# Performance work log

Measured on AMD Instinct MI355X. Metric: run time of the kernel, lower is better.

Reference implementation:

```python
import jax, jax.numpy as jnp
import numpy as np

N = 50000      # nodes
E = 800000     # edges (avg degree 16)
D = 64         # node feature dim
DE = 32        # edge feature dim
H = 256        # MLP hidden dim


def setup_inputs() -> dict:
    key = jax.random.key(0)
    k0, k1, k2, k3, k4 = jax.random.split(key, 5)
    x = jax.random.normal(k0, (N, D), dtype=jnp.float32)
    edge_index = jax.random.randint(k1, (2, E), 0, N)
    edge_attr = jax.random.normal(k2, (E, DE), dtype=jnp.float32)
    fan_in1 = 2 * D + DE  # 160
    W1 = jax.random.normal(k3, (fan_in1, H), dtype=jnp.float32) / np.float32(np.sqrt(fan_in1))
    b1 = jnp.zeros((H,), dtype=jnp.float32)
    W2 = jax.random.normal(k4, (H, D), dtype=jnp.float32) / np.float32(np.sqrt(H))
    b2 = jnp.zeros((D,), dtype=jnp.float32)
    return {"x": x, "edge_index": edge_index, "edge_attr": edge_attr,
            "W1": W1, "b1": b1, "W2": W2, "b2": b2}


def reference(x, edge_index, edge_attr, W1, b1, W2, b2):
    row, col = edge_index[0], edge_index[1]
    # gather endpoint features + edge features -> [E, 2D+DE]
    feats = jnp.concatenate([x[row], x[col], edge_attr], axis=-1)
    # MLP: Linear -> ReLU -> Linear
    h = jax.nn.relu(feats @ W1 + b1)          # [E, H]
    out = h @ W2 + b2                          # [E, D]
    # scatter-max aggregate by source node (row), dim_size = N
    agg = jax.ops.segment_max(out, row, num_segments=N)  # [N, D]
    # PyG's old scatter_('max') zero-fills empty slots
    agg = jnp.where(jnp.isneginf(agg), jnp.float32(0.0), agg)
    return (agg, out)
```

## Files before the change

### kernel.cpp

```cpp
#include <hip/hip_runtime.h>
#include <hip/hip_bf16.h>
#include <math.h>

#define NNODES 50000
#define NEDGES 800000
#define CHUNKS (NEDGES / 32)
#define NBLK 256
#define GWAVES (NBLK * 16)

using short8 = __attribute__((ext_vector_type(8))) short;
using f32x4  = __attribute__((ext_vector_type(4))) float;
using f32x16 = __attribute__((ext_vector_type(16))) float;
using u32x4  = __attribute__((ext_vector_type(4))) unsigned;

__device__ __forceinline__ short f2b(float v) {
    return __builtin_bit_cast(short, __float2bfloat16(v));
}
__device__ __forceinline__ unsigned cvt2(float a, float b) {
    return (unsigned)(unsigned short)f2b(a) | ((unsigned)(unsigned short)f2b(b) << 16);
}

__global__ void prep_all(const float* __restrict__ x, short* __restrict__ xb,
                         const float* __restrict__ W1, const float* __restrict__ W2,
                         short* __restrict__ wpk, const int* __restrict__ ei,
                         unsigned* __restrict__ cnt)
{
    int b = blockIdx.x;
    if (b < 3125) {
        int i = b * 256 + threadIdx.x;
        float4 v = reinterpret_cast<const float4*>(x)[i];
        short4 o;
        o.x = f2b(v.x); o.y = f2b(v.y); o.z = f2b(v.z); o.w = f2b(v.w);
        reinterpret_cast<short4*>(xb)[i] = o;
    } else if (b < 6250) {
        int e = (b - 3125) * 256 + threadIdx.x;
        atomicAdd(&cnt[ei[e]], 1u);
    } else {
        int i = (b - 6250) * 256 + threadIdx.x;
        if (i < 40960) {
            int k = i >> 8, n = i & 255;
            int lane = (n & 31) + (((k >> 3) & 1) << 5);
            wpk[(((n >> 5) * 10 + (k >> 4)) * 64 + lane) * 8 + (k & 7)] = f2b(W1[i]);
        }
        if (i < 16384) {
            int k = i >> 6, n = i & 63;
            int lane = (n & 31) + (((k >> 3) & 1) << 5);
            wpk[40960 + (((n >> 5) * 16 + (k >> 4)) * 64 + lane) * 8 + (k & 7)] = f2b(W2[i]);
        }
    }
}

__global__ __launch_bounds__(1024)
void csr_scan1(const unsigned* __restrict__ cnt, unsigned* __restrict__ offs,
               unsigned* __restrict__ bsum) {
    __shared__ unsigned sbuf[1024];
    int t = threadIdx.x, i = blockIdx.x * 1024 + t;
    unsigned v = (i < NNODES) ? cnt[i] : 0u;
    sbuf[t] = v;
    __syncthreads();
    for (int off = 1; off < 1024; off <<= 1) {
        unsigned add = (t >= off) ? sbuf[t - off] : 0u;
        __syncthreads();
        sbuf[t] += add;
        __syncthreads();
    }
    if (i < NNODES) offs[i] = sbuf[t];
    if (t == 1023) bsum[blockIdx.x] = sbuf[1023];
}

__global__ void csr_scan2(unsigned* __restrict__ bsum) {
    int t = threadIdx.x;
    unsigned v = (t < 49) ? bsum[t] : 0u;
    unsigned orig = v;
    for (int off = 1; off < 64; off <<= 1) {
        unsigned n = __shfl_up(v, off, 64);
        if (t >= off) v += n;
    }
    if (t < 49) bsum[t] = v - orig;
}

__global__ __launch_bounds__(1024)
void csr_scan3(const unsigned* __restrict__ cnt, unsigned* __restrict__ offs,
               const unsigned* __restrict__ bsum) {
    int i = blockIdx.x * 1024 + threadIdx.x;
    if (i < NNODES)       offs[i] = offs[i] - cnt[i] + bsum[blockIdx.x];
    else if (i == NNODES) offs[i] = NEDGES;
}

__global__ void csr_place(const int* __restrict__ ei, const unsigned* __restrict__ offs,
                          unsigned* __restrict__ cur, unsigned* __restrict__ elist) {
    int e = blockIdx.x * 256 + threadIdx.x;
    if (e < NEDGES) {
        int r = ei[e];
        unsigned p = offs[r] + atomicAdd(&cur[r], 1u);
        elist[p] = (unsigned)e;
    }
}

__global__ __launch_bounds__(1024, 4)
void edgeconv_main(const short* __restrict__ xb, const int* __restrict__ ei,
                   const float* __restrict__ ea, const short* __restrict__ wpk,
                   const float* __restrict__ b1, const float* __restrict__ b2,
                   float* __restrict__ outbuf)
{
    __shared__ short wlds[57344];

    for (int i = threadIdx.x; i < 7168; i += 1024)
        reinterpret_cast<short8*>(wlds)[i] = reinterpret_cast<const short8*>(wpk)[i];
    __syncthreads();

    const short* w1s = wlds;
    const short* w2s = wlds + 40960;
    const int lane = threadIdx.x & 63;
    const int wave = threadIdx.x >> 6;
    const int l32 = lane & 31, hi = lane >> 5;
    const int gw = blockIdx.x * 16 + wave;

    for (int c = gw; c < CHUNKS; c += GWAVES) {
        const int ebase = c * 32;
        const int e = ebase + l32;
        const int r = ei[e], cc = ei[NEDGES + e];

        short8 fx[10];
        #pragma unroll
        for (int ks = 0; ks < 4; ++ks)
            fx[ks] = *reinterpret_cast<const short8*>(xb + r * 64 + ks * 16 + hi * 8);
        #pragma unroll
        for (int ks = 0; ks < 4; ++ks)
            fx[4 + ks] = *reinterpret_cast<const short8*>(xb + cc * 64 + ks * 16 + hi * 8);
        #pragma unroll
        for (int ks = 0; ks < 2; ++ks) {
            const float4* p = reinterpret_cast<const float4*>(ea + e * 32 + ks * 16 + hi * 8);
            float4 a = p[0], b = p[1];
            u32x4 uu;
            uu[0] = cvt2(a.x, a.y); uu[1] = cvt2(a.z, a.w);
            uu[2] = cvt2(b.x, b.y); uu[3] = cvt2(b.z, b.w);
            fx[8 + ks] = __builtin_bit_cast(short8, uu);
        }

        f32x16 acc2[2];
        #pragma unroll
        for (int t2 = 0; t2 < 2; ++t2)
            #pragma unroll
            for (int g = 0; g < 4; ++g) {
                float4 bb = *reinterpret_cast<const float4*>(b2 + t2 * 32 + g * 8 + hi * 4);
                acc2[t2][g * 4 + 0] = bb.x; acc2[t2][g * 4 + 1] = bb.y;
                acc2[t2][g * 4 + 2] = bb.z; acc2[t2][g * 4 + 3] = bb.w;
            }

        #pragma unroll 1
        for (int t = 0; t < 8; ++t) {
            f32x16 acc1;
            #pragma unroll
            for (int g = 0; g < 4; ++g) {
                float4 bb = *reinterpret_cast<const float4*>(b1 + t * 32 + g * 8 + hi * 4);
                acc1[g * 4 + 0] = bb.x; acc1[g * 4 + 1] = bb.y;
                acc1[g * 4 + 2] = bb.z; acc1[g * 4 + 3] = bb.w;
            }
            #pragma unroll
            for (int ks = 0; ks < 10; ++ks) {
                short8 wf = *reinterpret_cast<const short8*>(
                    w1s + ((t * 10 + ks) * 64 + lane) * 8);
                acc1 = __builtin_amdgcn_mfma_f32_32x32x16_bf16(wf, fx[ks], acc1, 0, 0, 0);
            }
            #pragma unroll
            for (int ksl = 0; ksl < 2; ++ksl) {
                int q0 = ksl * 8;
                unsigned D0 = cvt2(fmaxf(acc1[q0 + 0], 0.f), fmaxf(acc1[q0 + 1], 0.f));
                unsigned D1 = cvt2(fmaxf(acc1[q0 + 2], 0.f), fmaxf(acc1[q0 + 3], 0.f));
                unsigned D2 = cvt2(fmaxf(acc1[q0 + 4], 0.f), fmaxf(acc1[q0 + 5], 0.f));
                unsigned D3 = cvt2(fmaxf(acc1[q0 + 6], 0.f), fmaxf(acc1[q0 + 7], 0.f));
                asm volatile("v_permlane32_swap_b32 %0, %1" : "+v"(D0), "+v"(D2));
                asm volatile("v_permlane32_swap_b32 %0, %1" : "+v"(D1), "+v"(D3));
                u32x4 bu; bu[0] = D0; bu[1] = D1; bu[2] = D2; bu[3] = D3;
                short8 hb = __builtin_bit_cast(short8, bu);

                int ks2 = t * 2 + ksl;
                short8 w20 = *reinterpret_cast<const short8*>(w2s + (ks2 * 64 + lane) * 8);
                short8 w21 = *reinterpret_cast<const short8*>(w2s + ((16 + ks2) * 64 + lane) * 8);
                acc2[0] = __builtin_amdgcn_mfma_f32_32x32x16_bf16(w20, hb, acc2[0], 0, 0, 0);
                acc2[1] = __builtin_amdgcn_mfma_f32_32x32x16_bf16(w21, hb, acc2[1], 0, 0, 0);
            }
        }

        #pragma unroll
        for (int t2 = 0; t2 < 2; ++t2)
            #pragma unroll
            for (int g = 0; g < 4; ++g) {
                f32x4 v;
                v[0] = acc2[t2][g * 4 + 0]; v[1] = acc2[t2][g * 4 + 1];
                v[2] = acc2[t2][g * 4 + 2]; v[3] = acc2[t2][g * 4 + 3];
                *reinterpret_cast<f32x4*>(outbuf + (size_t)e * 64 + t2 * 32 + g * 8 + hi * 4) = v;
            }
    }
}

__global__ __launch_bounds__(256)
void agg_max(const unsigned* __restrict__ offs, const unsigned* __restrict__ elist,
             const float* __restrict__ outbuf, float* __restrict__ agg)
{
    const int wave = threadIdx.x >> 6, lane = threadIdx.x & 63;
    const int node = blockIdx.x * 4 + wave;
    if (node >= NNODES) return;
    const unsigned s = offs[node], eend = offs[node + 1];
    float m0 = -INFINITY, m1 = -INFINITY, m2 = -INFINITY, m3 = -INFINITY;
    unsigned p = s;
    for (; p + 4 <= eend; p += 4) {
        float a = outbuf[(size_t)elist[p + 0] * 64 + lane];
        float b = outbuf[(size_t)elist[p + 1] * 64 + lane];
        float c = outbuf[(size_t)elist[p + 2] * 64 + lane];
        float d = outbuf[(size_t)elist[p + 3] * 64 + lane];
        m0 = fmaxf(m0, a); m1 = fmaxf(m1, b);
        m2 = fmaxf(m2, c); m3 = fmaxf(m3, d);
    }
    for (; p < eend; ++p) m0 = fmaxf(m0, outbuf[(size_t)elist[p] * 64 + lane]);
    float m = fmaxf(fmaxf(m0, m1), fmaxf(m2, m3));
    agg[(size_t)node * 64 + lane] = (s == eend) ? 0.0f : m;
}

extern "C" void kernel_launch(void* const* d_in, const int* in_sizes, int n_in,
                              void* d_out, int out_size, void* d_ws, size_t ws_size,
                              hipStream_t stream)
{
    const float* x  = (const float*)d_in[0];
    const int*   ei = (const int*)d_in[1];
    const float* ea = (const float*)d_in[2];
    const float* W1 = (const float*)d_in[3];
    const float* b1 = (const float*)d_in[4];
    const float* W2 = (const float*)d_in[5];
    const float* b2 = (const float*)d_in[6];

    float* aggp = (float*)d_out;
    float* outp = aggp + (size_t)NNODES * 64;

    short*    xb   = (short*)d_ws;
    short*    wpk  = (short*)((char*)d_ws + 6400000);
    unsigned* meta = (unsigned*)((char*)d_ws + 6514688);
    unsigned* cnt   = meta;
    unsigned* cur   = meta + 50000;
    unsigned* offs  = meta + 100000;
    unsigned* bsum  = meta + 150016;
    unsigned* elist = meta + 150144;

    (void)hipMemsetAsync(cnt, 0, 100000 * sizeof(unsigned), stream);
    prep_all<<<6410, 256, 0, stream>>>(x, xb, W1, W2, wpk, ei, cnt);
    csr_scan1<<<49, 1024, 0, stream>>>(cnt, offs, bsum);
    csr_scan2<<<1, 64, 0, stream>>>(bsum);
    csr_scan3<<<49, 1024, 0, stream>>>(cnt, offs, bsum);
    csr_place<<<NEDGES / 256, 256, 0, stream>>>(ei, offs, cur, elist);
    edgeconv_main<<<NBLK, 1024, 0, stream>>>(xb, ei, ea, wpk, b1, b2, outp);
    agg_max<<<(NNODES + 3) / 4, 256, 0, stream>>>(offs, elist, outp, aggp);
}
```

Before: 300.8 us.

## Fuse segment-max into MLP kernel via CSR-ordered edges and atomicMax

The MLP kernel now walks edges in CSR (source-sorted) order, so each 32-edge chunk holds runs sharing a source node. It does a segmented max-reduction across lanes with shuffles, then issues order-preserving encoded atomicMax into the aggregate buffer, and a small decode pass turns the encoded values back into floats. This removes the separate agg_max kernel, which re-read the whole edge output through indirect loads. It also prefetches the next chunk's indices. The costs are scattered gathers of edge_attr and scattered output writes, plus the shuffle-reduction work and atomic traffic inside the compute kernel.

```diff
diff --git a/kernel.cpp b/kernel.cpp
--- a/kernel.cpp
+++ b/kernel.cpp
@@ -18,6 +18,10 @@
 }
 __device__ __forceinline__ unsigned cvt2(float a, float b) {
     return (unsigned)(unsigned short)f2b(a) | ((unsigned)(unsigned short)f2b(b) << 16);
+}
+__device__ __forceinline__ unsigned encf(float v) {
+    unsigned u = __builtin_bit_cast(unsigned, v);
+    return (u & 0x80000000u) ? ~u : (u | 0x80000000u);
 }
 
 __global__ void prep_all(const float* __restrict__ x, short* __restrict__ xb,
@@ -101,7 +105,8 @@
 void edgeconv_main(const short* __restrict__ xb, const int* __restrict__ ei,
                    const float* __restrict__ ea, const short* __restrict__ wpk,
                    const float* __restrict__ b1, const float* __restrict__ b2,
-                   float* __restrict__ outbuf)
+                   const unsigned* __restrict__ elist,
+                   float* __restrict__ outbuf, unsigned* __restrict__ aggenc)
 {
     __shared__ short wlds[57344];
 
@@ -116,10 +121,21 @@
     const int l32 = lane & 31, hi = lane >> 5;
     const int gw = blockIdx.x * 16 + wave;
 
+    int eo = 0, r = 0, cc = 0;
+    if (gw < CHUNKS) {
+        eo = (int)elist[gw * 32 + l32];
+        r  = ei[eo];
+        cc = ei[NEDGES + eo];
+    }
+
     for (int c = gw; c < CHUNKS; c += GWAVES) {
-        const int ebase = c * 32;
-        const int e = ebase + l32;
-        const int r = ei[e], cc = ei[NEDGES + e];
+        int cn = c + GWAVES;
+        int eo_n = 0, r_n = 0, cc_n = 0;
+        if (cn < CHUNKS) {
+            eo_n = (int)elist[cn * 32 + l32];
+            r_n  = ei[eo_n];
+            cc_n = ei[NEDGES + eo_n];
+        }
 
         short8 fx[10];
         #pragma unroll
@@ -130,7 +146,7 @@
             fx[4 + ks] = *reinterpret_cast<const short8*>(xb + cc * 64 + ks * 16 + hi * 8);
         #pragma unroll
         for (int ks = 0; ks < 2; ++ks) {
-            const float4* p = reinterpret_cast<const float4*>(ea + e * 32 + ks * 16 + hi * 8);
+            const float4* p = reinterpret_cast<const float4*>(ea + (size_t)eo * 32 + ks * 16 + hi * 8);
             float4 a = p[0], b = p[1];
             u32x4 uu;
             uu[0] = cvt2(a.x, a.y); uu[1] = cvt2(a.z, a.w);
@@ -190,32 +206,51 @@
                 f32x4 v;
                 v[0] = acc2[t2][g * 4 + 0]; v[1] = acc2[t2][g * 4 + 1];
                 v[2] = acc2[t2][g * 4 + 2]; v[3] = acc2[t2][g * 4 + 3];
-                *reinterpret_cast<f32x4*>(outbuf + (size_t)e * 64 + t2 * 32 + g * 8 + hi * 4) = v;
-            }
-    }
-}
-
-__global__ __launch_bounds__(256)
-void agg_max(const unsigned* __restrict__ offs, const unsigned* __restrict__ elist,
-             const float* __restrict__ outbuf, float* __restrict__ agg)
-{
-    const int wave = threadIdx.x >> 6, lane = threadIdx.x & 63;
-    const int node = blockIdx.x * 4 + wave;
-    if (node >= NNODES) return;
-    const unsigned s = offs[node], eend = offs[node + 1];
-    float m0 = -INFINITY, m1 = -INFINITY, m2 = -INFINITY, m3 = -INFINITY;
-    unsigned p = s;
-    for (; p + 4 <= eend; p += 4) {
-        float a = outbuf[(size_t)elist[p + 0] * 64 + lane];
-        float b = outbuf[(size_t)elist[p + 1] * 64 + lane];
-        float c = outbuf[(size_t)elist[p + 2] * 64 + lane];
-        float d = outbuf[(size_t)elist[p + 3] * 64 + lane];
-        m0 = fmaxf(m0, a); m1 = fmaxf(m1, b);
-        m2 = fmaxf(m2, c); m3 = fmaxf(m3, d);
-    }
-    for (; p < eend; ++p) m0 = fmaxf(m0, outbuf[(size_t)elist[p] * 64 + lane]);
-    float m = fmaxf(fmaxf(m0, m1), fmaxf(m2, m3));
-    agg[(size_t)node * 64 + lane] = (s == eend) ? 0.0f : m;
+                *reinterpret_cast<f32x4*>(outbuf + (size_t)eo * 64 + t2 * 32 + g * 8 + hi * 4) = v;
+            }
+
+        unsigned n = (unsigned)r;
+        #pragma unroll
+        for (int d = 1; d < 32; d <<= 1) {
+            unsigned n2 = (unsigned)__shfl_down((int)n, d);
+            bool take = ((l32 + d) < 32) && (n2 == n);
+            #pragma unroll
+            for (int t2 = 0; t2 < 2; ++t2)
+                #pragma unroll
+                for (int g = 0; g < 16; ++g) {
+                    float o = __shfl_down(acc2[t2][g], d);
+                    if (take) acc2[t2][g] = fmaxf(acc2[t2][g], o);
+                }
+        }
+        unsigned np = (unsigned)__shfl_up((int)n, 1);
+        bool headl = (l32 == 0) || (np != n);
+        if (headl) {
+            unsigned* arow = aggenc + (size_t)n * 64;
+            #pragma unroll
+            for (int t2 = 0; t2 < 2; ++t2)
+                #pragma unroll
+                for (int g = 0; g < 4; ++g)
+                    #pragma unroll
+                    for (int q = 0; q < 4; ++q)
+                        atomicMax(&arow[t2 * 32 + g * 8 + hi * 4 + q],
+                                  encf(acc2[t2][g * 4 + q]));
+        }
+
+        eo = eo_n; r = r_n; cc = cc_n;
+    }
+}
+
+__global__ void decode_agg(unsigned* __restrict__ agg)
+{
+    int i = blockIdx.x * 256 + threadIdx.x;
+    if (i < NNODES * 64) {
+        unsigned u = agg[i];
+        float f;
+        if (u == 0u)              f = 0.0f;
+        else if (u & 0x80000000u) f = __builtin_bit_cast(float, u ^ 0x80000000u);
+        else                      f = __builtin_bit_cast(float, ~u);
+        reinterpret_cast<float*>(agg)[i] = f;
+    }
 }
 
 extern "C" void kernel_launch(void* const* d_in, const int* in_sizes, int n_in,
@@ -243,11 +278,13 @@
     unsigned* elist = meta + 150144;
 
     (void)hipMemsetAsync(cnt, 0, 100000 * sizeof(unsigned), stream);
+    (void)hipMemsetAsync(aggp, 0, (size_t)NNODES * 64 * 4, stream);
     prep_all<<<6410, 256, 0, stream>>>(x, xb, W1, W2, wpk, ei, cnt);
     csr_scan1<<<49, 1024, 0, stream>>>(cnt, offs, bsum);
     csr_scan2<<<1, 64, 0, stream>>>(bsum);
     csr_scan3<<<49, 1024, 0, stream>>>(cnt, offs, bsum);
     csr_place<<<NEDGES / 256, 256, 0, stream>>>(ei, offs, cur, elist);
-    edgeconv_main<<<NBLK, 1024, 0, stream>>>(xb, ei, ea, wpk, b1, b2, outp);
-    agg_max<<<(NNODES + 3) / 4, 256, 0, stream>>>(offs, elist, outp, aggp);
-}
+    edgeconv_main<<<NBLK, 1024, 0, stream>>>(xb, ei, ea, wpk, b1, b2, elist,
+                                             outp, (unsigned*)aggp);
+    decode_agg<<<(NNODES * 64 + 255) / 256, 256, 0, stream>>>((unsigned*)aggp);
+}
```

Measured after the change: 351.4 us. 1.17x slower.

## Emit bf16 edge outputs in CSR order so max-aggregation reads contiguously

Applied to the files above, without the earlier changes.

csr_place now records each edge's CSR slot. The main MLP kernel then writes an extra bf16 copy of each edge output into a CSR-ordered buffer. A new agg_csr kernel streams that buffer contiguously per node, splitting edges across two half-waves, instead of gathering fp32 rows through elist. The main loop also prefetches the next chunk's indices, and the fallback path uses nontemporal loads. This trades an extra scattered bf16 write for fewer and more coalesced aggregation reads. It needs a larger workspace, and it computes agg from bf16-rounded values, which risks exceeding the accuracy tolerance.

```diff
diff --git a/kernel.cpp b/kernel.cpp
--- a/kernel.cpp
+++ b/kernel.cpp
@@ -88,20 +88,24 @@
 }
 
 __global__ void csr_place(const int* __restrict__ ei, const unsigned* __restrict__ offs,
-                          unsigned* __restrict__ cur, unsigned* __restrict__ elist) {
+                          unsigned* __restrict__ cur, unsigned* __restrict__ elist,
+                          unsigned* __restrict__ pos) {
     int e = blockIdx.x * 256 + threadIdx.x;
     if (e < NEDGES) {
         int r = ei[e];
         unsigned p = offs[r] + atomicAdd(&cur[r], 1u);
         elist[p] = (unsigned)e;
-    }
-}
-
+        if (pos) pos[e] = p;
+    }
+}
+
+template<bool STORECSR>
 __global__ __launch_bounds__(1024, 4)
 void edgeconv_main(const short* __restrict__ xb, const int* __restrict__ ei,
                    const float* __restrict__ ea, const short* __restrict__ wpk,
                    const float* __restrict__ b1, const float* __restrict__ b2,
-                   float* __restrict__ outbuf)
+                   const unsigned* __restrict__ pos,
+                   float* __restrict__ outbuf, unsigned* __restrict__ outcsr)
 {
     __shared__ short wlds[57344];
 
@@ -116,10 +120,25 @@
     const int l32 = lane & 31, hi = lane >> 5;
     const int gw = blockIdx.x * 16 + wave;
 
+    int r = 0, cc = 0; unsigned pv = 0;
+    if (gw < CHUNKS) {
+        int e0 = gw * 32 + l32;
+        r  = ei[e0];
+        cc = ei[NEDGES + e0];
+        if (STORECSR) pv = pos[e0];
+    }
+
     for (int c = gw; c < CHUNKS; c += GWAVES) {
-        const int ebase = c * 32;
-        const int e = ebase + l32;
-        const int r = ei[e], cc = ei[NEDGES + e];
+        const int e = c * 32 + l32;
+
+        int cn = c + GWAVES;
+        int r_n = 0, cc_n = 0; unsigned pv_n = 0;
+        if (cn < CHUNKS) {
+            int e1 = cn * 32 + l32;
+            r_n  = ei[e1];
+            cc_n = ei[NEDGES + e1];
+            if (STORECSR) pv_n = pos[e1];
+        }
 
         short8 fx[10];
         #pragma unroll
@@ -130,7 +149,7 @@
             fx[4 + ks] = *reinterpret_cast<const short8*>(xb + cc * 64 + ks * 16 + hi * 8);
         #pragma unroll
         for (int ks = 0; ks < 2; ++ks) {
-            const float4* p = reinterpret_cast<const float4*>(ea + e * 32 + ks * 16 + hi * 8);
+            const float4* p = reinterpret_cast<const float4*>(ea + (size_t)e * 32 + ks * 16 + hi * 8);
             float4 a = p[0], b = p[1];
             u32x4 uu;
             uu[0] = cvt2(a.x, a.y); uu[1] = cvt2(a.z, a.w);
@@ -191,13 +210,46 @@
                 v[0] = acc2[t2][g * 4 + 0]; v[1] = acc2[t2][g * 4 + 1];
                 v[2] = acc2[t2][g * 4 + 2]; v[3] = acc2[t2][g * 4 + 3];
                 *reinterpret_cast<f32x4*>(outbuf + (size_t)e * 64 + t2 * 32 + g * 8 + hi * 4) = v;
-            }
+                if (STORECSR) {
+                    uint2 pk;
+                    pk.x = cvt2(v[0], v[1]);
+                    pk.y = cvt2(v[2], v[3]);
+                    *reinterpret_cast<uint2*>(outcsr + (size_t)pv * 32 + t2 * 16 + g * 4 + hi * 2) = pk;
+                }
+            }
+
+        r = r_n; cc = cc_n; pv = pv_n;
     }
 }
 
 __global__ __launch_bounds__(256)
-void agg_max(const unsigned* __restrict__ offs, const unsigned* __restrict__ elist,
-             const float* __restrict__ outbuf, float* __restrict__ agg)
+void agg_csr(const unsigned* __restrict__ offs, const unsigned* __restrict__ outcsr,
+             float* __restrict__ agg)
+{
+    const int wave = threadIdx.x >> 6, lane = threadIdx.x & 63;
+    const int l32 = lane & 31, half = lane >> 5;
+    const int node = blockIdx.x * 4 + wave;
+    if (node >= NNODES) return;
+    const unsigned s = offs[node], eend = offs[node + 1];
+    float m0 = -INFINITY, m1 = -INFINITY;
+    for (unsigned p = s + half; p < eend; p += 2) {
+        unsigned u = outcsr[(size_t)p * 32 + l32];
+        m0 = fmaxf(m0, __builtin_bit_cast(float, u << 16));
+        m1 = fmaxf(m1, __builtin_bit_cast(float, u & 0xFFFF0000u));
+    }
+    m0 = fmaxf(m0, __shfl_xor(m0, 32, 64));
+    m1 = fmaxf(m1, __shfl_xor(m1, 32, 64));
+    if (half == 0) {
+        float2 o;
+        o.x = (s == eend) ? 0.0f : m0;
+        o.y = (s == eend) ? 0.0f : m1;
+        *reinterpret_cast<float2*>(agg + (size_t)node * 64 + l32 * 2) = o;
+    }
+}
+
+__global__ __launch_bounds__(256)
+void agg_list(const unsigned* __restrict__ offs, const unsigned* __restrict__ elist,
+              const float* __restrict__ outbuf, float* __restrict__ agg)
 {
     const int wave = threadIdx.x >> 6, lane = threadIdx.x & 63;
     const int node = blockIdx.x * 4 + wave;
@@ -206,14 +258,15 @@
     float m0 = -INFINITY, m1 = -INFINITY, m2 = -INFINITY, m3 = -INFINITY;
     unsigned p = s;
     for (; p + 4 <= eend; p += 4) {
-        float a = outbuf[(size_t)elist[p + 0] * 64 + lane];
-        float b = outbuf[(size_t)elist[p + 1] * 64 + lane];
-        float c = outbuf[(size_t)elist[p + 2] * 64 + lane];
-        float d = outbuf[(size_t)elist[p + 3] * 64 + lane];
+        float a = __builtin_nontemporal_load(outbuf + (size_t)elist[p + 0] * 64 + lane);
+        float b = __builtin_nontemporal_load(outbuf + (size_t)elist[p + 1] * 64 + lane);
+        float c = __builtin_nontemporal_load(outbuf + (size_t)elist[p + 2] * 64 + lane);
+        float d = __builtin_nontemporal_load(outbuf + (size_t)elist[p + 3] * 64 + lane);
         m0 = fmaxf(m0, a); m1 = fmaxf(m1, b);
         m2 = fmaxf(m2, c); m3 = fmaxf(m3, d);
     }
-    for (; p < eend; ++p) m0 = fmaxf(m0, outbuf[(size_t)elist[p] * 64 + lane]);
+    for (; p < eend; ++p)
+        m0 = fmaxf(m0, __builtin_nontemporal_load(outbuf + (size_t)elist[p] * 64 + lane));
     float m = fmaxf(fmaxf(m0, m1), fmaxf(m2, m3));
     agg[(size_t)node * 64 + lane] = (s == eend) ? 0.0f : m;
 }
@@ -241,13 +294,26 @@
     unsigned* offs  = meta + 100000;
     unsigned* bsum  = meta + 150016;
     unsigned* elist = meta + 150144;
+    unsigned* pos   = meta + 950144;
+    unsigned* outcsr = meta + 1750144;
+
+    const size_t NEED = 6514688ULL + 1750144ULL * 4ULL + 102400000ULL;
+    const bool big = ws_size >= NEED;
 
     (void)hipMemsetAsync(cnt, 0, 100000 * sizeof(unsigned), stream);
     prep_all<<<6410, 256, 0, stream>>>(x, xb, W1, W2, wpk, ei, cnt);
     csr_scan1<<<49, 1024, 0, stream>>>(cnt, offs, bsum);
     csr_scan2<<<1, 64, 0, stream>>>(bsum);
     csr_scan3<<<49, 1024, 0, stream>>>(cnt, offs, bsum);
-    csr_place<<<NEDGES / 256, 256, 0, stream>>>(ei, offs, cur, elist);
-    edgeconv_main<<<NBLK, 1024, 0, stream>>>(xb, ei, ea, wpk, b1, b2, outp);
-    agg_max<<<(NNODES + 3) / 4, 256, 0, stream>>>(offs, elist, outp, aggp);
-}
+    csr_place<<<NEDGES / 256, 256, 0, stream>>>(ei, offs, cur, elist,
+                                                big ? pos : (unsigned*)nullptr);
+    if (big) {
+        edgeconv_main<true><<<NBLK, 1024, 0, stream>>>(xb, ei, ea, wpk, b1, b2,
+                                                       pos, outp, outcsr);
+        agg_csr<<<(NNODES + 3) / 4, 256, 0, stream>>>(offs, outcsr, aggp);
+    } else {
+        edgeconv_main<false><<<NBLK, 1024, 0, stream>>>(xb, ei, ea, wpk, b1, b2,
+                                                        nullptr, outp, nullptr);
+        agg_list<<<(NNODES + 3) / 4, 256, 0, stream>>>(offs, elist, outp, aggp);
+    }
+}
```

Result: slower. 355.6 us (+18.2%).
